# Performance work log

Measured on AMD Instinct MI355X. Metric: run time of the kernel, lower is better.

The kernel has to match this reference:

```python
import jax, jax.numpy as jnp
import numpy as np

B, T, I, H, O = 1024, 512, 64, 256, 1

def setup_inputs() -> dict:
    key = jax.random.key(0)
    ks = jax.random.split(key, 12)
    s_ih0 = 1.0 / np.sqrt(H)
    def u(k, shape):
        return jax.random.uniform(k, shape, jnp.float32, -s_ih0, s_ih0)
    return {
        "x": jax.random.normal(ks[0], (B, T, I), jnp.float32),
        "w_ih0": u(ks[1], (4 * H, I)),
        "w_hh0": u(ks[2], (4 * H, H)),
        "b_ih0": u(ks[3], (4 * H,)),
        "b_hh0": u(ks[4], (4 * H,)),
        "w_ih1": u(ks[5], (4 * H, H)),
        "w_hh1": u(ks[6], (4 * H, H)),
        "b_ih1": u(ks[7], (4 * H,)),
        "b_hh1": u(ks[8], (4 * H,)),
        "fc_w": u(ks[9], (O, H)),
        "fc_b": u(ks[10], (O,)),
    }

def _lstm_layer(x, w_ih, w_hh, b_ih, b_hh):
    # x: [B, T, D_in] -> hidden sequence [B, T, H], gate order i,f,g,o (PyTorch)
    b, t, _ = x.shape
    h_dim = w_hh.shape[1]
    # precompute input projections for all timesteps: [T, B, 4H]
    xproj = (jnp.einsum('bti,gi->btg', x, w_ih) + b_ih + b_hh).transpose(1, 0, 2)
    h0 = jnp.zeros((b, h_dim), x.dtype)
    c0 = jnp.zeros((b, h_dim), x.dtype)

    def step(carry, xp):
        h, c = carry
        gates = xp + h @ w_hh.T  # [B, 4H]
        i_g, f_g, g_g, o_g = jnp.split(gates, 4, axis=-1)
        i_g = jax.nn.sigmoid(i_g)
        f_g = jax.nn.sigmoid(f_g)
        g_g = jnp.tanh(g_g)
        o_g = jax.nn.sigmoid(o_g)
        c = f_g * c + i_g * g_g
        h = o_g * jnp.tanh(c)
        return (h, c), h

    (h_last, _), hs = jax.lax.scan(step, (h0, c0), xproj)
    return hs.transpose(1, 0, 2), h_last

def reference(x, w_ih0, w_hh0, b_ih0, b_hh0, w_ih1, w_hh1, b_ih1, b_hh1, fc_w, fc_b):
    # Layer 0 -> (eval mode: dropout is identity) -> Layer 1 -> fc on last step
    h_seq0, _ = _lstm_layer(x, w_ih0, w_hh0, b_ih0, b_hh0)
    _, h_last1 = _lstm_layer(h_seq0, w_ih1, w_hh1, b_ih1, b_hh1)
    return h_last1 @ fc_w.T + fc_b  # [B, O]
```

## Files before the change

kernel.cpp:

```cpp
#include <hip/hip_runtime.h>
#include <stdint.h>


#define T_STEPS 512
#define NC0 10
#define NC1 16
#define WSLICE_ELEMS (4*(NC0+NC1)*512)
#define L1_OFF (4*NC0*512)
#define HN (1024*256)

typedef __attribute__((ext_vector_type(8))) short short8;
typedef __attribute__((ext_vector_type(4))) float floatx4;
typedef __attribute__((ext_vector_type(4))) int   intx4;
typedef _Float16 half8 __attribute__((ext_vector_type(8)));

#define MFMA16(A,B,C) __builtin_amdgcn_mfma_f32_16x16x32_f16( \
    __builtin_bit_cast(half8,(A)), __builtin_bit_cast(half8,(B)), (C), 0, 0, 0)

__device__ __forceinline__ float sigm(float x){
  return __builtin_amdgcn_rcpf(1.0f + __builtin_amdgcn_exp2f(-1.44269504f*x));
}
__device__ __forceinline__ float tanhf_(float x){
  return 1.0f - 2.0f*__builtin_amdgcn_rcpf(1.0f + __builtin_amdgcn_exp2f(2.88539008f*x));
}
__device__ __forceinline__ floatx4 splat4(float v){ return (floatx4){v,v,v,v}; }
__device__ __forceinline__ int imin2(int a, int b){ return a < b ? a : b; }

__device__ __forceinline__ void cvt8h(const floatx4& v0, const floatx4& v1, short8& hi, short8& lo){
  #pragma unroll
  for (int j = 0; j < 8; ++j){
    float f = (j < 4) ? v0[j] : v1[j-4];
    _Float16 h = (_Float16)f;
    _Float16 l = (_Float16)(f - (float)h);
    hi[j] = (short)__builtin_bit_cast(uint16_t, h);
    lo[j] = (short)__builtin_bit_cast(uint16_t, l);
  }
}

__device__ __forceinline__ short8 load_coh16(const uint16_t* p){
  short8 r;
  asm volatile("global_load_dwordx4 %0, %1, off sc0 sc1" : "=v"(r) : "v"(p));
  return r;
}
__device__ __forceinline__ void store_coh2(uint16_t* p, uint32_t v){
  asm volatile("global_store_short %0, %1, off sc0 sc1" :: "v"(p), "v"(v) : "memory");
}
__device__ __forceinline__ floatx4 load_g16f(const float* p){
  floatx4 r;
  asm volatile("global_load_dwordx4 %0, %1, off" : "=v"(r) : "v"(p));
  return r;
}
__device__ __forceinline__ void flag_store(int* p, int v){
  asm volatile("global_store_dword %0, %1, off sc0 sc1" :: "v"(p), "v"(v) : "memory");
}
__device__ __forceinline__ intx4 load_flags4(const int* p){
  intx4 r;
  asm volatile("global_load_dwordx4 %0, %1, off sc0 sc1" : "=v"(r) : "v"(p));
  return r;
}
#define VM_WAIT(N) do{ asm volatile("s_waitcnt vmcnt(" #N ")" ::: "memory"); \
                       __builtin_amdgcn_sched_barrier(0); }while(0)

__device__ __forceinline__ void poll_flags(const int* f, int target){
  int spins = 0;
  for(;;){
    intx4 a = load_flags4(f);
    intx4 b = load_flags4(f + 4);
    intx4 c = load_flags4(f + 8);
    intx4 d = load_flags4(f + 12);
    VM_WAIT(0);
    int m = imin2(imin2(a[0],a[1]), imin2(a[2],a[3]));
    m = imin2(m, imin2(imin2(b[0],b[1]), imin2(b[2],b[3])));
    m = imin2(m, imin2(imin2(c[0],c[1]), imin2(c[2],c[3])));
    m = imin2(m, imin2(imin2(d[0],d[1]), imin2(d[2],d[3])));
    if (m >= target) break;
    if (++spins > (1<<20)) break;
    __builtin_amdgcn_s_sleep(1);
  }
  __builtin_amdgcn_sched_barrier(0);
}

extern "C" __global__ void prep_weights(const float* __restrict__ wih0, const float* __restrict__ whh0,
                                        const float* __restrict__ wih1, const float* __restrict__ whh1,
                                        uint16_t* __restrict__ wfrag)
{
  int idx = blockIdx.x*256 + threadIdx.x;
  int s  = idx / WSLICE_ELEMS;
  int r  = idx - s*WSLICE_ELEMS;
  int layer = (r >= L1_OFF) ? 1 : 0;
  int rr = layer ? (r - L1_OFF) : r;
  int nc = layer ? NC1 : NC0;
  int n  = rr / (nc*512);
  int c  = (rr / 512) % nc;
  int l  = (rr >> 3) & 63;
  int j  = rr & 7;
  int k  = c*32 + ((l >> 4) << 3) + j;
  int grow = n*256 + s*16 + (l & 15);
  float v;
  if (!layer) v = (k < 64)  ? wih0[grow*64  + k] : whh0[grow*256 + (k - 64)];
  else        v = (k < 256) ? wih1[grow*256 + k] : whh1[grow*256 + (k - 256)];
  wfrag[idx] = __builtin_bit_cast(uint16_t, (_Float16)v);
}

extern "C" __global__ void prep_bias(const float* __restrict__ bih0, const float* __restrict__ bhh0,
                                     const float* __restrict__ bih1, const float* __restrict__ bhh1,
                                     float* __restrict__ biasg)
{
  int idx = blockIdx.x*256 + threadIdx.x;
  if (idx >= 16*2*64) return;
  int s = idx >> 7;
  int layer = (idx >> 6) & 1;
  int q = idx & 63;
  int grow = (q >> 4)*256 + s*16 + (q & 15);
  biasg[idx] = layer ? (bih1[grow] + bhh1[grow]) : (bih0[grow] + bhh0[grow]);
}

extern "C" __global__ void __launch_bounds__(256, 1)
lstm_main(const float* __restrict__ x,
          const uint16_t* __restrict__ wfrag,
          const float* __restrict__ biasg,
          uint16_t* __restrict__ hbase,
          const float* __restrict__ fcw,
          const float* __restrict__ fcb,
          int* __restrict__ flg,
          float* __restrict__ out)
{
  extern __shared__ uint16_t wlds[];
  const int tid  = threadIdx.x;
  const int bid  = blockIdx.x;
  const int s    = bid >> 4;
  const int g    = bid & 15;
  const int wv   = tid >> 6;
  const int lane = tid & 63;

  const int arow = g*64 + wv*16 + (lane & 15);
  const int ka   = (lane >> 4) * 8;
  const int drow = g*64 + wv*16 + ((lane >> 4) << 2);
  const int dcol = s*16 + (lane & 15);

  {
    const uint16_t* wsrc = wfrag + (size_t)s*WSLICE_ELEMS;
    for (int i = tid*8; i < WSLICE_ELEMS; i += 256*8)
      *(short8*)(wlds + i) = *(const short8*)(wsrc + i);
  }
  float b0[4], b1[4];
  {
    const int col = lane & 15;
    #pragma unroll
    for (int n = 0; n < 4; ++n){
      b0[n] = biasg[(s*2+0)*64 + n*16 + col];
      b1[n] = biasg[(s*2+1)*64 + n*16 + col];
    }
  }
  const float fcwv = fcw[dcol];
  const float fcb0 = fcb[0];
  __syncthreads();

  const uint16_t* wl = wlds + lane*8;
  const size_t abase = (size_t)arow*256 + ka;
  float c0[4] = {0,0,0,0}, c1[4] = {0,0,0,0};
  int* f0 = flg + g*64;
  int* f1 = flg + 1024 + g*64;

  short8 xh[2], xl[2];
  {
    const float* xp = x + (size_t)arow*T_STEPS*64 + ka;
    floatx4 v0 = *(const floatx4*)(xp);
    floatx4 v1 = *(const floatx4*)(xp + 4);
    floatx4 v2 = *(const floatx4*)(xp + 32);
    floatx4 v3 = *(const floatx4*)(xp + 36);
    cvt8h(v0, v1, xh[0], xl[0]);
    cvt8h(v2, v3, xh[1], xl[1]);
  }
  short8 k1h[8], k1l[8];
  {
    const uint16_t* ph = hbase + 4*(size_t)HN + abase;
    const uint16_t* pl = hbase + 6*(size_t)HN + abase;
    #pragma unroll
    for (int kc = 0; kc < 8; ++kc){
      k1h[kc] = load_coh16(ph + kc*32);
      k1l[kc] = load_coh16(pl + kc*32);
    }
    VM_WAIT(0);
  }

  for (int t = 0; t < T_STEPS; ++t){
    const size_t par0  = (size_t)(t & 1);
    const size_t rpar0 = par0 ^ 1;

    poll_flags(f0, t);

    short8 a0h[8], a0l[8];
    {
      const uint16_t* ph = hbase + rpar0*HN + abase;
      const uint16_t* pl = hbase + 2*(size_t)HN + rpar0*HN + abase;
      #pragma unroll
      for (int kc = 0; kc < 8; ++kc) a0h[kc] = load_coh16(ph + kc*32);
      #pragma unroll
      for (int kc = 0; kc < 8; ++kc) a0l[kc] = load_coh16(pl + kc*32);
    }
    floatx4 xr0, xr1, xr2, xr3;
    {
      const int tn = (t < T_STEPS-1) ? (t+1) : t;
      const float* xp = x + ((size_t)arow*T_STEPS + tn)*64 + ka;
      xr0 = load_g16f(xp);      xr1 = load_g16f(xp + 4);
      xr2 = load_g16f(xp + 32); xr3 = load_g16f(xp + 36);
    }

    floatx4 acc0[4], acc1[4];
    #pragma unroll
    for (int n = 0; n < 4; ++n){ acc0[n] = splat4(b0[n]); acc1[n] = splat4(b1[n]); }
    #pragma unroll
    for (int kc = 0; kc < 8; ++kc){
      #pragma unroll
      for (int n = 0; n < 4; ++n){
        short8 w = *(const short8*)(wl + L1_OFF + (n*NC1 + 8 + kc)*512);
        acc1[n] = MFMA16(k1h[kc], w, acc1[n]);
        acc1[n] = MFMA16(k1l[kc], w, acc1[n]);
      }
    }
    #pragma unroll
    for (int pk = 0; pk < 2; ++pk){
      #pragma unroll
      for (int n = 0; n < 4; ++n){
        short8 w = *(const short8*)(wl + (n*NC0 + pk)*512);
        acc0[n] = MFMA16(xh[pk], w, acc0[n]);
        acc0[n] = MFMA16(xl[pk], w, acc0[n]);
      }
    }

    VM_WAIT(4);

    #pragma unroll
    for (int kc = 0; kc < 8; ++kc){
      #pragma unroll
      for (int n = 0; n < 4; ++n){
        short8 w0 = *(const short8*)(wl + (n*NC0 + 2 + kc)*512);
        acc0[n] = MFMA16(a0h[kc], w0, acc0[n]);
        acc0[n] = MFMA16(a0l[kc], w0, acc0[n]);
        short8 w1 = *(const short8*)(wl + L1_OFF + (n*NC1 + kc)*512);
        acc1[n] = MFMA16(a0h[kc], w1, acc1[n]);
        acc1[n] = MFMA16(a0l[kc], w1, acc1[n]);
      }
    }

    {
      uint16_t* qh = hbase + par0*HN;
      uint16_t* ql = hbase + 2*(size_t)HN + par0*HN;
      #pragma unroll
      for (int r = 0; r < 4; ++r){
        float ig = sigm(acc0[0][r]);
        float fg = sigm(acc0[1][r]);
        float gg = tanhf_(acc0[2][r]);
        float og = sigm(acc0[3][r]);
        c0[r] = fg*c0[r] + ig*gg;
        float h = og*tanhf_(c0[r]);
        _Float16 hh = (_Float16)h;
        _Float16 hl = (_Float16)(h - (float)hh);
        size_t idx = (size_t)(drow + r)*256 + dcol;
        store_coh2(qh + idx, (uint32_t)__builtin_bit_cast(uint16_t, hh));
        store_coh2(ql + idx, (uint32_t)__builtin_bit_cast(uint16_t, hl));
      }
    }
    VM_WAIT(0);
    __syncthreads();
    if (tid == 0) flag_store(f0 + s, t+1);

    cvt8h(xr0, xr1, xh[0], xl[0]);
    cvt8h(xr2, xr3, xh[1], xl[1]);

    if (t > 0){
      uint16_t* qh = hbase + 4*(size_t)HN + rpar0*HN;
      uint16_t* ql = hbase + 6*(size_t)HN + rpar0*HN;
      #pragma unroll
      for (int r = 0; r < 4; ++r){
        float ig = sigm(acc1[0][r]);
        float fg = sigm(acc1[1][r]);
        float gg = tanhf_(acc1[2][r]);
        float og = sigm(acc1[3][r]);
        c1[r] = fg*c1[r] + ig*gg;
        float h = og*tanhf_(c1[r]);
        _Float16 hh = (_Float16)h;
        _Float16 hl = (_Float16)(h - (float)hh);
        size_t idx = (size_t)(drow + r)*256 + dcol;
        store_coh2(qh + idx, (uint32_t)__builtin_bit_cast(uint16_t, hh));
        store_coh2(ql + idx, (uint32_t)__builtin_bit_cast(uint16_t, hl));
      }
    }
    VM_WAIT(0);
    __syncthreads();
    if (tid == 0) flag_store(f1 + s, t+1);

    poll_flags(f1, t+1);
    {
      const uint16_t* ph = hbase + 4*(size_t)HN + rpar0*HN + abase;
      const uint16_t* pl = hbase + 6*(size_t)HN + rpar0*HN + abase;
      #pragma unroll
      for (int kc = 0; kc < 8; ++kc){
        k1h[kc] = load_coh16(ph + kc*32);
        k1l[kc] = load_coh16(pl + kc*32);
      }
    }
  }

  {
    const uint16_t* p0h = hbase + 1*(size_t)HN + abase;
    const uint16_t* p0l = hbase + 3*(size_t)HN + abase;
    short8 a0h[8], a0l[8];
    #pragma unroll
    for (int kc = 0; kc < 8; ++kc){
      a0h[kc] = load_coh16(p0h + kc*32);
      a0l[kc] = load_coh16(p0l + kc*32);
    }
    VM_WAIT(0);
    floatx4 acc[4];
    #pragma unroll
    for (int n = 0; n < 4; ++n) acc[n] = splat4(b1[n]);
    #pragma unroll
    for (int kc = 0; kc < 8; ++kc){
      #pragma unroll
      for (int n = 0; n < 4; ++n){
        short8 w1 = *(const short8*)(wl + L1_OFF + (n*NC1 + kc)*512);
        acc[n] = MFMA16(a0h[kc], w1, acc[n]);
        acc[n] = MFMA16(a0l[kc], w1, acc[n]);
        short8 w2 = *(const short8*)(wl + L1_OFF + (n*NC1 + 8 + kc)*512);
        acc[n] = MFMA16(k1h[kc], w2, acc[n]);
        acc[n] = MFMA16(k1l[kc], w2, acc[n]);
      }
    }
    #pragma unroll
    for (int r = 0; r < 4; ++r){
      float ig = sigm(acc[0][r]);
      float fg = sigm(acc[1][r]);
      float gg = tanhf_(acc[2][r]);
      float og = sigm(acc[3][r]);
      float cc = fg*c1[r] + ig*gg;
      float h  = og*tanhf_(cc);
      float v  = h * fcwv;
      v += __shfl_xor(v, 1);
      v += __shfl_xor(v, 2);
      v += __shfl_xor(v, 4);
      v += __shfl_xor(v, 8);
      if ((lane & 15) == 0){
        float res = v + ((s == 0) ? fcb0 : 0.0f);
        atomicAdd(out + drow + r, res);
      }
    }
  }
}

extern "C" void kernel_launch(void* const* d_in, const int* in_sizes, int n_in,
                              void* d_out, int out_size, void* d_ws, size_t ws_size,
                              hipStream_t stream)
{
  (void)in_sizes; (void)n_in; (void)out_size; (void)ws_size;
  const float* x    = (const float*)d_in[0];
  const float* wih0 = (const float*)d_in[1];
  const float* whh0 = (const float*)d_in[2];
  const float* bih0 = (const float*)d_in[3];
  const float* bhh0 = (const float*)d_in[4];
  const float* wih1 = (const float*)d_in[5];
  const float* whh1 = (const float*)d_in[6];
  const float* bih1 = (const float*)d_in[7];
  const float* bhh1 = (const float*)d_in[8];
  const float* fcw  = (const float*)d_in[9];
  const float* fcb  = (const float*)d_in[10];

  char* ws = (char*)d_ws;
  const size_t SZ_WFRAG = (size_t)16*WSLICE_ELEMS*2;
  const size_t OFF_BIAS = SZ_WFRAG;
  const size_t OFF_FLG  = OFF_BIAS + (size_t)16*2*64*4;
  const size_t OFF_H    = (size_t)2*1024*1024;

  uint16_t* wfrag = (uint16_t*)(ws);
  float*    biasg = (float*)(ws + OFF_BIAS);
  int*      flg   = (int*)(ws + OFF_FLG);
  uint16_t* hbase = (uint16_t*)(ws + OFF_H);
  float*    out   = (float*)d_out;

  hipMemsetAsync(d_out, 0, (size_t)1024*sizeof(float), stream);
  hipMemsetAsync(ws + OFF_FLG, 0, (OFF_H - OFF_FLG) + (size_t)8*HN*2, stream);

  hipLaunchKernelGGL(prep_weights, dim3(16*WSLICE_ELEMS/256), dim3(256), 0, stream,
                     wih0, whh0, wih1, whh1, wfrag);
  hipLaunchKernelGGL(prep_bias, dim3(8), dim3(256), 0, stream,
                     bih0, bhh0, bih1, bhh1, biasg);

  hipFuncSetAttribute((const void*)lstm_main,
                      hipFuncAttributeMaxDynamicSharedMemorySize, WSLICE_ELEMS*2);
  void* args[] = { (void*)&x, (void*)&wfrag, (void*)&biasg, (void*)&hbase,
                   (void*)&fcw, (void*)&fcb, (void*)&flg, (void*)&out };
  hipError_t ce = hipLaunchCooperativeKernel((void*)lstm_main, dim3(256), dim3(256),
                                             args, WSLICE_ELEMS*2, stream);
  if (ce != hipSuccess){
    hipLaunchKernelGGL(lstm_main, dim3(256), dim3(256), WSLICE_ELEMS*2, stream,
                       x, wfrag, biasg, hbase, fcw, fcb, flg, out);
  }
}
```

Baseline: 4.971 ms.

## Merge layer-0 and layer-1 barriers into a single flag per timestep

Removes the second flag barrier (f1) for layer 1. Each step now publishes one flag after both layers' hidden stores, and the layer-1 hidden state is loaded from the previous parity buffer alongside the layer-0 loads, after the single poll. A staggered s_sleep per group is added before the loop to spread out polling contention. This halves the cross-block synchronisation per step but lengthens the loads at the start of each step. It also relies on the parity buffers keeping layer-1 results consistent across the reordering.

```diff
diff --git a/kernel.cpp b/kernel.cpp
--- a/kernel.cpp
+++ b/kernel.cpp
@@ -160,7 +160,6 @@
   const size_t abase = (size_t)arow*256 + ka;
   float c0[4] = {0,0,0,0}, c1[4] = {0,0,0,0};
   int* f0 = flg + g*64;
-  int* f1 = flg + 1024 + g*64;
 
   short8 xh[2], xl[2];
   {
@@ -172,17 +171,8 @@
     cvt8h(v0, v1, xh[0], xl[0]);
     cvt8h(v2, v3, xh[1], xl[1]);
   }
-  short8 k1h[8], k1l[8];
-  {
-    const uint16_t* ph = hbase + 4*(size_t)HN + abase;
-    const uint16_t* pl = hbase + 6*(size_t)HN + abase;
-    #pragma unroll
-    for (int kc = 0; kc < 8; ++kc){
-      k1h[kc] = load_coh16(ph + kc*32);
-      k1l[kc] = load_coh16(pl + kc*32);
-    }
-    VM_WAIT(0);
-  }
+
+  for (int i = 0; i < g*6; ++i) __builtin_amdgcn_s_sleep(2);
 
   for (int t = 0; t < T_STEPS; ++t){
     const size_t par0  = (size_t)(t & 1);
@@ -190,7 +180,15 @@
 
     poll_flags(f0, t);
 
-    short8 a0h[8], a0l[8];
+    short8 a1h[8], a1l[8], a0h[8], a0l[8];
+    {
+      const uint16_t* ph = hbase + 4*(size_t)HN + par0*HN + abase;
+      const uint16_t* pl = hbase + 6*(size_t)HN + par0*HN + abase;
+      #pragma unroll
+      for (int kc = 0; kc < 8; ++kc) a1h[kc] = load_coh16(ph + kc*32);
+      #pragma unroll
+      for (int kc = 0; kc < 8; ++kc) a1l[kc] = load_coh16(pl + kc*32);
+    }
     {
       const uint16_t* ph = hbase + rpar0*HN + abase;
       const uint16_t* pl = hbase + 2*(size_t)HN + rpar0*HN + abase;
@@ -211,21 +209,24 @@
     #pragma unroll
     for (int n = 0; n < 4; ++n){ acc0[n] = splat4(b0[n]); acc1[n] = splat4(b1[n]); }
     #pragma unroll
-    for (int kc = 0; kc < 8; ++kc){
-      #pragma unroll
-      for (int n = 0; n < 4; ++n){
-        short8 w = *(const short8*)(wl + L1_OFF + (n*NC1 + 8 + kc)*512);
-        acc1[n] = MFMA16(k1h[kc], w, acc1[n]);
-        acc1[n] = MFMA16(k1l[kc], w, acc1[n]);
-      }
-    }
-    #pragma unroll
     for (int pk = 0; pk < 2; ++pk){
       #pragma unroll
       for (int n = 0; n < 4; ++n){
         short8 w = *(const short8*)(wl + (n*NC0 + pk)*512);
         acc0[n] = MFMA16(xh[pk], w, acc0[n]);
         acc0[n] = MFMA16(xl[pk], w, acc0[n]);
+      }
+    }
+
+    VM_WAIT(20);
+
+    #pragma unroll
+    for (int kc = 0; kc < 8; ++kc){
+      #pragma unroll
+      for (int n = 0; n < 4; ++n){
+        short8 w = *(const short8*)(wl + L1_OFF + (n*NC1 + 8 + kc)*512);
+        acc1[n] = MFMA16(a1h[kc], w, acc1[n]);
+        acc1[n] = MFMA16(a1l[kc], w, acc1[n]);
       }
     }
 
@@ -262,13 +263,6 @@
         store_coh2(ql + idx, (uint32_t)__builtin_bit_cast(uint16_t, hl));
       }
     }
-    VM_WAIT(0);
-    __syncthreads();
-    if (tid == 0) flag_store(f0 + s, t+1);
-
-    cvt8h(xr0, xr1, xh[0], xl[0]);
-    cvt8h(xr2, xr3, xh[1], xl[1]);
-
     if (t > 0){
       uint16_t* qh = hbase + 4*(size_t)HN + rpar0*HN;
       uint16_t* ql = hbase + 6*(size_t)HN + rpar0*HN;
@@ -287,30 +281,28 @@
         store_coh2(ql + idx, (uint32_t)__builtin_bit_cast(uint16_t, hl));
       }
     }
+
     VM_WAIT(0);
     __syncthreads();
-    if (tid == 0) flag_store(f1 + s, t+1);
-
-    poll_flags(f1, t+1);
-    {
-      const uint16_t* ph = hbase + 4*(size_t)HN + rpar0*HN + abase;
-      const uint16_t* pl = hbase + 6*(size_t)HN + rpar0*HN + abase;
-      #pragma unroll
-      for (int kc = 0; kc < 8; ++kc){
-        k1h[kc] = load_coh16(ph + kc*32);
-        k1l[kc] = load_coh16(pl + kc*32);
-      }
-    }
-  }
-
+    if (tid == 0) flag_store(f0 + s, t+1);
+
+    cvt8h(xr0, xr1, xh[0], xl[0]);
+    cvt8h(xr2, xr3, xh[1], xl[1]);
+  }
+
+  poll_flags(f0, T_STEPS);
   {
     const uint16_t* p0h = hbase + 1*(size_t)HN + abase;
     const uint16_t* p0l = hbase + 3*(size_t)HN + abase;
-    short8 a0h[8], a0l[8];
+    const uint16_t* p1h = hbase + 4*(size_t)HN + abase;
+    const uint16_t* p1l = hbase + 6*(size_t)HN + abase;
+    short8 a0h[8], a0l[8], a1h[8], a1l[8];
     #pragma unroll
     for (int kc = 0; kc < 8; ++kc){
       a0h[kc] = load_coh16(p0h + kc*32);
       a0l[kc] = load_coh16(p0l + kc*32);
+      a1h[kc] = load_coh16(p1h + kc*32);
+      a1l[kc] = load_coh16(p1l + kc*32);
     }
     VM_WAIT(0);
     floatx4 acc[4];
@@ -324,8 +316,8 @@
         acc[n] = MFMA16(a0h[kc], w1, acc[n]);
         acc[n] = MFMA16(a0l[kc], w1, acc[n]);
         short8 w2 = *(const short8*)(wl + L1_OFF + (n*NC1 + 8 + kc)*512);
-        acc[n] = MFMA16(k1h[kc], w2, acc[n]);
-        acc[n] = MFMA16(k1l[kc], w2, acc[n]);
+        acc[n] = MFMA16(a1h[kc], w2, acc[n]);
+        acc[n] = MFMA16(a1l[kc], w2, acc[n]);
       }
     }
     #pragma unroll
```

Result: no change. 4.970 ms (-0.0%).
